# Optimization experiments

Measured on AMD Instinct MI355X. Metric: run time of the kernel, lower is better.

The kernel has to match this reference:

```python
import jax, jax.numpy as jnp
import numpy as np

BOUND = 2.0


def _near_far_cube(rays_o, rays_d, bound):
    tmin = (-bound - rays_o) / (rays_d + 1e-15)
    tmax = (bound - rays_o) / (rays_d + 1e-15)
    near = jnp.max(jnp.minimum(tmin, tmax), axis=-1, keepdims=True)
    far = jnp.min(jnp.maximum(tmin, tmax), axis=-1, keepdims=True)
    bad = far < near
    near = jnp.where(bad, 1e9, near)
    far = jnp.where(bad, 1e9, far)
    near = jnp.maximum(near, 0.05)
    return near, far


def _sample_pdf_det(bins, weights, n_samples):
    # bins: [R, M], weights: [R, M-1]  (deterministic / eval-mode u)
    weights = weights + 1e-5
    pdf = weights / jnp.sum(weights, -1, keepdims=True)
    cdf = jnp.cumsum(pdf, -1)
    cdf = jnp.concatenate([jnp.zeros_like(cdf[:, :1]), cdf], -1)  # [R, M]
    u = jnp.linspace(0.5 / n_samples, 1.0 - 0.5 / n_samples, n_samples, dtype=cdf.dtype)
    u = jnp.broadcast_to(u, (cdf.shape[0], n_samples))
    inds = jax.vmap(lambda c, uu: jnp.searchsorted(c, uu, side='right'))(cdf, u)
    below = jnp.maximum(inds - 1, 0)
    above = jnp.minimum(inds, cdf.shape[-1] - 1)
    cdf_b = jnp.take_along_axis(cdf, below, -1)
    cdf_a = jnp.take_along_axis(cdf, above, -1)
    bins_b = jnp.take_along_axis(bins, below, -1)
    bins_a = jnp.take_along_axis(bins, above, -1)
    denom = cdf_a - cdf_b
    denom = jnp.where(denom < 1e-5, jnp.ones_like(denom), denom)
    t = (u - cdf_b) / denom
    return bins_b + t * (bins_a - bins_b)


def _field(pts, dirs, W1, b1, W2, b2, Wsig, Wrgb, brgb):
    # stand-in NeRF field (base class is abstract): tiny MLP
    h = jax.nn.relu(pts @ W1 + b1)
    h = jax.nn.relu(h @ W2 + b2)
    sigma = jax.nn.softplus((h @ Wsig)[..., 0])
    rgb = jax.nn.sigmoid(jnp.concatenate([h, dirs], -1) @ Wrgb + brgb)
    return sigma, rgb


def _composite_weights(z_vals, sigmas, sample_dist):
    deltas = z_vals[..., 1:] - z_vals[..., :-1]
    deltas = jnp.concatenate([deltas, jnp.broadcast_to(sample_dist, deltas[..., :1].shape)], -1)
    alphas = 1.0 - jnp.exp(-deltas * sigmas)
    shifted = jnp.concatenate([jnp.ones_like(alphas[..., :1]), 1.0 - alphas + 1e-15], -1)
    weights = alphas * jnp.cumprod(shifted, -1)[..., :-1]
    return weights, deltas


def _run(rays_o, rays_d, W1, b1, W2, b2, Wsig, Wrgb, brgb, num_steps, upsample_steps):
    B, N = rays_o.shape[:2]
    near, far = _near_far_cube(rays_o, rays_d, BOUND)          # [B,N,1]
    z = jnp.linspace(0.0, 1.0, num_steps, dtype=rays_o.dtype)
    z_vals = near + (far - near) * z                            # [B,N,S]
    sample_dist = (far - near) / num_steps                      # [B,N,1]
    pts = jnp.clip(rays_o[..., None, :] + rays_d[..., None, :] * z_vals[..., None], -BOUND, BOUND)
    dirs = jnp.broadcast_to(rays_d[..., None, :], pts.shape)
    sigmas, rgbs = _field(pts, dirs, W1, b1, W2, b2, Wsig, Wrgb, brgb)  # [B,N,S], [B,N,S,3]

    # importance resampling (no_grad + detach in torch -> stop_gradient)
    w, deltas = _composite_weights(z_vals, sigmas, sample_dist)
    z_mid = z_vals[..., :-1] + 0.5 * deltas[..., :-1]           # [B,N,S-1]
    new_z = _sample_pdf_det(z_mid.reshape(B * N, -1), w.reshape(B * N, -1)[:, 1:-1], upsample_steps)
    new_z = jax.lax.stop_gradient(new_z).reshape(B, N, upsample_steps)
    new_pts = jnp.clip(rays_o[..., None, :] + rays_d[..., None, :] * new_z[..., None], -BOUND, BOUND)
    new_dirs = jnp.broadcast_to(rays_d[..., None, :], new_pts.shape)
    new_sigmas, new_rgbs = _field(new_pts, new_dirs, W1, b1, W2, b2, Wsig, Wrgb, brgb)

    # merge coarse + fine samples, sort along ray
    z_all = jnp.concatenate([z_vals, new_z], -1)                # [B,N,S+U]
    idx = jnp.argsort(z_all, axis=-1)
    z_all = jnp.take_along_axis(z_all, idx, -1)
    sig_all = jnp.take_along_axis(jnp.concatenate([sigmas, new_sigmas], -1), idx, -1)
    rgb_all = jnp.take_along_axis(jnp.concatenate([rgbs, new_rgbs], -2), idx[..., None], -2)

    w, _ = _composite_weights(z_all, sig_all, sample_dist)
    weights_sum = jnp.sum(w, -1)                                # [B,N]
    ori_z = jnp.clip((z_all - near) / (far - near), 0.0, 1.0)
    depth = jnp.sum(w * ori_z, -1)                              # [B,N]
    image = jnp.sum(w[..., None] * rgb_all, -2)                 # [B,N,3]
    image = image + (1.0 - weights_sum)[..., None] * 1.0        # bg_color = 1
    return depth, image


def setup_inputs() -> dict:
    key = jax.random.key(0)
    ks = jax.random.split(key, 8)
    B, N, H = 1, 4096, 64
    rays_o = jax.random.normal(ks[0], (B, N, 3), jnp.float32) * 0.5
    rays_d = jax.random.normal(ks[1], (B, N, 3), jnp.float32)
    rays_d = rays_d / jnp.linalg.norm(rays_d, axis=-1, keepdims=True)
    return {
        'rays_o': rays_o,
        'rays_d': rays_d,
        'W1': jax.random.normal(ks[2], (3, H), jnp.float32) / np.sqrt(3.0),
        'b1': jnp.zeros((H,), jnp.float32),
        'W2': jax.random.normal(ks[3], (H, H), jnp.float32) / np.sqrt(H),
        'b2': jnp.zeros((H,), jnp.float32),
        'Wsig': jax.random.normal(ks[4], (H, 1), jnp.float32) / np.sqrt(H),
        'Wrgb': jax.random.normal(ks[5], (H + 3, 3), jnp.float32) / np.sqrt(H + 3),
        'brgb': jnp.zeros((3,), jnp.float32),
        'num_steps': 128,
        'upsample_steps': 128,
    }


def reference(rays_o, rays_d, W1, b1, W2, b2, Wsig, Wrgb, brgb, num_steps, upsample_steps):
    return _run(rays_o, rays_d, W1, b1, W2, b2, Wsig, Wrgb, brgb, num_steps, upsample_steps)
```

## Files before the change

### kernel.cpp

```cpp
#include <hip/hip_runtime.h>
#include <math.h>


#define BOUNDF 2.0f

typedef _Float16 f16;
typedef f16 f16x2 __attribute__((ext_vector_type(2)));
typedef f16 f16x8 __attribute__((ext_vector_type(8)));
typedef float f32x4 __attribute__((ext_vector_type(4)));

union U16 { f16x8 v8; f16x2 v2[4]; };

struct RayLds {
    float zc[128];
    float zf[128];
    float sgc[128];
    float sgf[128];
    float rgbc[128][3];
    float rgbf[128][3];
    float cdf[128];
    float scr[128];
    unsigned short perm[256];
};

__device__ __forceinline__ f32x4 mfma16(f16x8 a, f16x8 b, f32x4 c) {
    return __builtin_amdgcn_mfma_f32_16x16x32_f16(a, b, c, 0, 0, 0);
}

__device__ __forceinline__ f16x2 pkrtz(float a, float b) {
    return __builtin_bit_cast(f16x2, __builtin_amdgcn_cvt_pkrtz(a, b));
}

__device__ __forceinline__ f16x8 relu_pk(f16x8 x) {
    const f16x8 z = {(f16)0.f, (f16)0.f, (f16)0.f, (f16)0.f,
                     (f16)0.f, (f16)0.f, (f16)0.f, (f16)0.f};
    return __builtin_elementwise_max(x, z);
}

__device__ __forceinline__ float scan_incl_mul(float p, int lane) {
#pragma unroll
    for (int off = 1; off < 64; off <<= 1) {
        float t = __shfl_up(p, off, 64);
        if (lane >= off) p *= t;
    }
    return p;
}

__device__ __forceinline__ float scan_incl_add(float p, int lane) {
#pragma unroll
    for (int off = 1; off < 64; off <<= 1) {
        float t = __shfl_up(p, off, 64);
        if (lane >= off) p += t;
    }
    return p;
}

template<bool COARSE>
__device__ __forceinline__ void field_pass(
    RayLds& R,
    f16x8 w1a0, f16x8 w1a1, f16x8 w1a2, f16x8 w1a3,
    f16x8 b00, f16x8 b01, f16x8 b10, f16x8 b11,
    f16x8 b20, f16x8 b21, f16x8 b30, f16x8 b31,
    f16x8 hda0, f16x8 hda1,
    f32x4 b2q0, f32x4 b2q1, f32x4 b2q2, f32x4 b2q3,
    float ox, float oy, float oz, float dx, float dy, float dzv,
    float nearv, float span, float base_r, float base_g, float base_b, int lane)
{
    const int ms = lane & 15;
    f32x4* stage = (f32x4*)(&R.cdf[0]);
    const f32x4 zero = {0.f, 0.f, 0.f, 0.f};
    U16 up;
    up.v2[2] = f16x2{(f16)0.f, (f16)0.f};
    up.v2[3] = f16x2{(f16)0.f, (f16)0.f};
#pragma unroll 1
    for (int Mtb = 0; Mtb < 2; ++Mtb) {
#pragma unroll 2
        for (int Mti = 0; Mti < 4; ++Mti) {
            int m = Mtb * 64 + Mti * 16 + ms;
            float z = COARSE ? fmaf(span, (float)m * (1.0f / 127.0f), nearv) : R.zf[m];
            float px = fminf(fmaxf(fmaf(dx, z, ox), -BOUNDF), BOUNDF);
            float py = fminf(fmaxf(fmaf(dy, z, oy), -BOUNDF), BOUNDF);
            float pz = fminf(fmaxf(fmaf(dzv, z, oz), -BOUNDF), BOUNDF);

            up.v2[0] = pkrtz(px, py);
            up.v2[1] = pkrtz(pz, 1.0f);
            f16x8 pf = up.v8;

            f32x4 hacc0 = mfma16(w1a0, pf, zero);
            f32x4 hacc1 = mfma16(w1a1, pf, zero);
            f32x4 hacc2 = mfma16(w1a2, pf, zero);
            f32x4 hacc3 = mfma16(w1a3, pf, zero);

            U16 u0, u1;
            u0.v2[0] = pkrtz(hacc0[0], hacc0[1]);
            u0.v2[1] = pkrtz(hacc0[2], hacc0[3]);
            u0.v2[2] = pkrtz(hacc1[0], hacc1[1]);
            u0.v2[3] = pkrtz(hacc1[2], hacc1[3]);
            u1.v2[0] = pkrtz(hacc2[0], hacc2[1]);
            u1.v2[1] = pkrtz(hacc2[2], hacc2[3]);
            u1.v2[2] = pkrtz(hacc3[0], hacc3[1]);
            u1.v2[3] = pkrtz(hacc3[2], hacc3[3]);
            f16x8 hf0 = relu_pk(u0.v8), hf1 = relu_pk(u1.v8);

            f32x4 acc0 = mfma16(b01, hf1, mfma16(b00, hf0, b2q0));
            f32x4 acc1 = mfma16(b11, hf1, mfma16(b10, hf0, b2q1));
            f32x4 acc2 = mfma16(b21, hf1, mfma16(b20, hf0, b2q2));
            f32x4 acc3 = mfma16(b31, hf1, mfma16(b30, hf0, b2q3));

            U16 v0, v1;
            v0.v2[0] = pkrtz(acc0[0], acc0[1]);
            v0.v2[1] = pkrtz(acc0[2], acc0[3]);
            v0.v2[2] = pkrtz(acc1[0], acc1[1]);
            v0.v2[3] = pkrtz(acc1[2], acc1[3]);
            v1.v2[0] = pkrtz(acc2[0], acc2[1]);
            v1.v2[1] = pkrtz(acc2[2], acc2[3]);
            v1.v2[2] = pkrtz(acc3[0], acc3[1]);
            v1.v2[3] = pkrtz(acc3[2], acc3[3]);
            f16x8 h0 = relu_pk(v0.v8), h1f = relu_pk(v1.v8);

            f32x4 tv = mfma16(hda1, h1f, mfma16(hda0, h0, zero));
            if (lane < 16) stage[Mti * 16 + ms] = tv;
        }
        {
            f32x4 tq = stage[lane];
            int m2 = Mtb * 64 + lane;
            float e  = __expf(-fabsf(tq[0]));
            float sg = fmaxf(tq[0], 0.0f) + __logf(1.0f + e);
            float rr = __builtin_amdgcn_rcpf(1.0f + __expf(-(tq[1] + base_r)));
            float gg = __builtin_amdgcn_rcpf(1.0f + __expf(-(tq[2] + base_g)));
            float bb = __builtin_amdgcn_rcpf(1.0f + __expf(-(tq[3] + base_b)));
            if (COARSE) {
                R.sgc[m2] = sg;
                R.rgbc[m2][0] = rr; R.rgbc[m2][1] = gg; R.rgbc[m2][2] = bb;
            } else {
                R.sgf[m2] = sg;
                R.rgbf[m2][0] = rr; R.rgbf[m2][1] = gg; R.rgbf[m2][2] = bb;
            }
        }
    }
}

__global__ __launch_bounds__(256)
void nerf_kernel(const float* __restrict__ rays_o, const float* __restrict__ rays_d,
                 const float* __restrict__ W1, const float* __restrict__ b1,
                 const float* __restrict__ W2, const float* __restrict__ b2,
                 const float* __restrict__ Wsig, const float* __restrict__ Wrgb,
                 const float* __restrict__ brgb,
                 float* __restrict__ out_depth, float* __restrict__ out_img,
                 int nRays)
{
    __shared__ RayLds rl[4];

    const int tid  = threadIdx.x;
    const int lane = tid & 63;
    const int wv   = tid >> 6;
    const int ms   = lane & 15;
    const int quad = lane >> 4;

    f16x8 w1a[4];
#pragma unroll
    for (int nt = 0; nt < 4; ++nt) {
        f16x8 t;
#pragma unroll
        for (int j = 0; j < 8; ++j) t[j] = (f16)0.f;
        if (quad == 0) {
            int u = 32 * (nt >> 1) + 8 * (ms >> 2) + 4 * (nt & 1) + (ms & 3);
            t[0] = (f16)W1[u];
            t[1] = (f16)W1[64 + u];
            t[2] = (f16)W1[128 + u];
            t[3] = (f16)b1[u];
        }
        w1a[nt] = t;
    }

    const int colbase = 8 * (ms >> 2) + (ms & 3);
    f16x8 b00, b01, b10, b11, b20, b21, b30, b31;
#pragma unroll
    for (int j = 0; j < 8; ++j) {
        int k0 = (quad * 8 + j) * 64;
        int k1 = (32 + quad * 8 + j) * 64;
        b00[j] = (f16)W2[k0 + colbase];      b01[j] = (f16)W2[k1 + colbase];
        b10[j] = (f16)W2[k0 + colbase + 4];  b11[j] = (f16)W2[k1 + colbase + 4];
        b20[j] = (f16)W2[k0 + colbase + 32]; b21[j] = (f16)W2[k1 + colbase + 32];
        b30[j] = (f16)W2[k0 + colbase + 36]; b31[j] = (f16)W2[k1 + colbase + 36];
    }
    f32x4 b2q0, b2q1, b2q2, b2q3;
#pragma unroll
    for (int r = 0; r < 4; ++r) {
        b2q0[r] = b2[8 * quad + r];
        b2q1[r] = b2[8 * quad + 4 + r];
        b2q2[r] = b2[32 + 8 * quad + r];
        b2q3[r] = b2[32 + 8 * quad + 4 + r];
    }
    f16x8 hda0, hda1;
    {
        int msel = ms & 3;
#pragma unroll
        for (int j = 0; j < 8; ++j) {
            int u0 = quad * 8 + j, u1 = 32 + quad * 8 + j;
            float w0 = (msel == 0) ? Wsig[u0] : Wrgb[u0 * 3 + msel - 1];
            float w1 = (msel == 0) ? Wsig[u1] : Wrgb[u1 * 3 + msel - 1];
            hda0[j] = (f16)w0;
            hda1[j] = (f16)w1;
        }
    }

    int ray = blockIdx.x * 4 + wv;
    bool valid = ray < nRays;
    int rayc = valid ? ray : (nRays - 1);
    RayLds& R = rl[wv];

    const float ox = rays_o[rayc * 3 + 0], oy = rays_o[rayc * 3 + 1], oz = rays_o[rayc * 3 + 2];
    const float dx = rays_d[rayc * 3 + 0], dy = rays_d[rayc * 3 + 1], dzv = rays_d[rayc * 3 + 2];

    float t0x = (-BOUNDF - ox) / (dx + 1e-15f), t1x = (BOUNDF - ox) / (dx + 1e-15f);
    float t0y = (-BOUNDF - oy) / (dy + 1e-15f), t1y = (BOUNDF - oy) / (dy + 1e-15f);
    float t0z = (-BOUNDF - oz) / (dzv + 1e-15f), t1z = (BOUNDF - oz) / (dzv + 1e-15f);
    float nearv = fmaxf(fminf(t0x, t1x), fmaxf(fminf(t0y, t1y), fminf(t0z, t1z)));
    float farv  = fminf(fmaxf(t0x, t1x), fminf(fmaxf(t0y, t1y), fmaxf(t0z, t1z)));
    if (farv < nearv) { nearv = 1e9f; farv = 1e9f; }
    nearv = fmaxf(nearv, 0.05f);
    const float span = farv - nearv;
    const float dzc = span * (1.0f / 127.0f);
    const float sample_dist = span * (1.0f / 128.0f);

    const float base_r = brgb[0] + dx * Wrgb[64 * 3 + 0] + dy * Wrgb[65 * 3 + 0] + dzv * Wrgb[66 * 3 + 0];
    const float base_g = brgb[1] + dx * Wrgb[64 * 3 + 1] + dy * Wrgb[65 * 3 + 1] + dzv * Wrgb[66 * 3 + 1];
    const float base_b = brgb[2] + dx * Wrgb[64 * 3 + 2] + dy * Wrgb[65 * 3 + 2] + dzv * Wrgb[66 * 3 + 2];

    const int s0 = lane, s1 = lane + 64;

    R.zc[s0] = fmaf(span, (float)s0 * (1.0f / 127.0f), nearv);
    R.zc[s1] = fmaf(span, (float)s1 * (1.0f / 127.0f), nearv);

    field_pass<true>(R, w1a[0], w1a[1], w1a[2], w1a[3],
                     b00, b01, b10, b11, b20, b21, b30, b31,
                     hda0, hda1, b2q0, b2q1, b2q2, b2q3,
                     ox, oy, oz, dx, dy, dzv, nearv, span, base_r, base_g, base_b, lane);

    {
        float zA = R.zc[s0], zB = R.zc[s1];
        float dA = R.zc[s0 + 1] - zA;
        float dB = (s1 < 127) ? (R.zc[s1 + 1] - zB) : sample_dist;
        R.scr[s0] = 1.0f - __expf(-dA * R.sgc[s0]);
        R.scr[s1] = 1.0f - __expf(-dB * R.sgc[s1]);
    }

    {
        float aa = R.scr[2 * lane], ab = R.scr[2 * lane + 1];
        float ma = 1.0f - aa + 1e-15f, mb = 1.0f - ab + 1e-15f;
        float p = scan_incl_mul(ma * mb, lane);
        float T0 = __shfl_up(p, 1, 64);
        if (lane == 0) T0 = 1.0f;
        R.scr[2 * lane]     = aa * T0;
        R.scr[2 * lane + 1] = ab * (T0 * ma);
    }

    {
        float pA = 0.f, pB = 0.f;
        if (lane < 63) {
            pA = R.scr[2 * lane + 1] + 1e-5f;
            pB = R.scr[2 * lane + 2] + 1e-5f;
        }
        float S = scan_incl_add(pA + pB, lane);
        float total = __shfl(S, 63, 64);
        float sexcl = __shfl_up(S, 1, 64);
        if (lane == 0) sexcl = 0.f;
        float inv = 1.0f / total;
        if (lane == 63) {
            R.cdf[0] = 0.0f;
        } else {
            R.cdf[1 + 2 * lane] = (sexcl + pA) * inv;
            R.cdf[2 + 2 * lane] = (sexcl + pA + pB) * inv;
        }
    }

#pragma unroll
    for (int bt = 0; bt < 2; ++bt) {
        int i = bt * 64 + lane;
        float u = (float)(2 * i + 1) * (1.0f / 256.0f);
        int lo = 0, hi = 127;
#pragma unroll
        for (int it = 0; it < 7; ++it) {
            int mid = (lo + hi) >> 1;
            if (R.cdf[mid] <= u) lo = mid + 1; else hi = mid;
        }
        int below = max(lo - 1, 0), above = min(lo, 126);
        float cb = R.cdf[below], ca = R.cdf[above];
        float binb = fmaf(dzc, (float)below + 0.5f, nearv);
        float bina = fmaf(dzc, (float)above + 0.5f, nearv);
        float denom = ca - cb;
        if (denom < 1e-5f) denom = 1.0f;
        float t = (u - cb) / denom;
        R.zf[i] = fmaf(t, bina - binb, binb);
    }

    field_pass<false>(R, w1a[0], w1a[1], w1a[2], w1a[3],
                      b00, b01, b10, b11, b20, b21, b30, b31,
                      hda0, hda1, b2q0, b2q1, b2q2, b2q3,
                      ox, oy, oz, dx, dy, dzv, nearv, span, base_r, base_g, base_b, lane);

#pragma unroll
    for (int bt = 0; bt < 2; ++bt) {
        int k = bt * 64 + lane;
        float v = R.zc[k];
        float vf = R.zf[k];
        int lo = 0, hi = 128;
        int lo2 = 0, hi2 = 128;
#pragma unroll
        for (int it = 0; it < 8; ++it) {
            if (lo < hi)   { int mid = (lo + hi) >> 1;   if (R.zf[mid] < v)   lo = mid + 1;  else hi = mid; }
            if (lo2 < hi2) { int mid = (lo2 + hi2) >> 1; if (R.zc[mid] <= vf) lo2 = mid + 1; else hi2 = mid; }
        }
        R.perm[k + lo]  = (unsigned short)k;
        R.perm[k + lo2] = (unsigned short)(128 + k);
    }

    {
        int sb = 4 * lane;
        int idxk[4]; float zk[4], sgk[4];
#pragma unroll
        for (int k = 0; k < 4; ++k) {
            int idx = R.perm[sb + k];
            idxk[k] = idx;
            zk[k]  = (idx < 128) ? R.zc[idx]  : R.zf[idx - 128];
            sgk[k] = (idx < 128) ? R.sgc[idx] : R.sgf[idx - 128];
        }
        float znext = __shfl_down(zk[0], 1, 64);
        float d0 = zk[1] - zk[0];
        float d1 = zk[2] - zk[1];
        float d2 = zk[3] - zk[2];
        float d3 = (lane < 63) ? (znext - zk[3]) : sample_dist;
        float a0 = 1.0f - __expf(-d0 * sgk[0]);
        float a1 = 1.0f - __expf(-d1 * sgk[1]);
        float a2 = 1.0f - __expf(-d2 * sgk[2]);
        float a3 = 1.0f - __expf(-d3 * sgk[3]);
        float m0 = 1.0f - a0 + 1e-15f, m1 = 1.0f - a1 + 1e-15f;
        float m2 = 1.0f - a2 + 1e-15f, m3 = 1.0f - a3 + 1e-15f;
        float p = scan_incl_mul((m0 * m1) * (m2 * m3), lane);
        float T = __shfl_up(p, 1, 64);
        if (lane == 0) T = 1.0f;

        const float invspan = 1.0f / span;
        float dacc = 0.f, racc = 0.f, gacc = 0.f, bacc = 0.f, wacc = 0.f;
        float aarr[4] = {a0, a1, a2, a3};
        float marr[4] = {m0, m1, m2, m3};
#pragma unroll
        for (int k = 0; k < 4; ++k) {
            float w = aarr[k] * T;
            float ozv = (zk[k] - nearv) * invspan;
            ozv = (ozv < 0.0f) ? 0.0f : ((ozv > 1.0f) ? 1.0f : ozv);
            dacc = fmaf(w, ozv, dacc);
            const float* rgb = (idxk[k] < 128) ? R.rgbc[idxk[k]] : R.rgbf[idxk[k] - 128];
            racc = fmaf(w, rgb[0], racc);
            gacc = fmaf(w, rgb[1], gacc);
            bacc = fmaf(w, rgb[2], bacc);
            wacc += w;
            T *= marr[k];
        }
#pragma unroll
        for (int off = 32; off; off >>= 1) {
            dacc += __shfl_xor(dacc, off);
            racc += __shfl_xor(racc, off);
            gacc += __shfl_xor(gacc, off);
            bacc += __shfl_xor(bacc, off);
            wacc += __shfl_xor(wacc, off);
        }
        if (lane == 0 && valid) {
            out_depth[ray] = dacc;
            float bg = 1.0f - wacc;
            out_img[ray * 3 + 0] = racc + bg;
            out_img[ray * 3 + 1] = gacc + bg;
            out_img[ray * 3 + 2] = bacc + bg;
        }
    }
}

extern "C" void kernel_launch(void* const* d_in, const int* in_sizes, int n_in,
                              void* d_out, int out_size, void* d_ws, size_t ws_size,
                              hipStream_t stream) {
    const float* rays_o = (const float*)d_in[0];
    const float* rays_d = (const float*)d_in[1];
    const float* W1   = (const float*)d_in[2];
    const float* b1   = (const float*)d_in[3];
    const float* W2   = (const float*)d_in[4];
    const float* b2   = (const float*)d_in[5];
    const float* Wsig = (const float*)d_in[6];
    const float* Wrgb = (const float*)d_in[7];
    const float* brgb = (const float*)d_in[8];

    int N = in_sizes[0] / 3;
    float* out = (float*)d_out;
    float* out_depth = out;
    float* out_img   = out + N;

    int blocks = (N + 3) / 4;
    nerf_kernel<<<dim3(blocks), dim3(256), 0, stream>>>(
        rays_o, rays_d, W1, b1, W2, b2, Wsig, Wrgb, brgb,
        out_depth, out_img, N);
}
```

Measured before the change: 98.59 us.

## Split each ray's field evaluation across two cooperating waves

Assigns two waves per ray instead of one. Each wave evaluates half of the coarse and fine MLP sample tiles, with block barriers before the stages that need all samples. Scan, CDF and composite stages are computed redundantly by both waves, with only one writing the output. This doubles wave-level parallelism to hide latency and raise occupancy, at the cost of duplicated serial work and extra barriers.

```diff
diff --git a/kernel.cpp b/kernel.cpp
--- a/kernel.cpp
+++ b/kernel.cpp
@@ -11,15 +11,17 @@
 
 union U16 { f16x8 v8; f16x2 v2[4]; };
 
-struct RayLds {
+struct __align__(16) RayLds {
     float zc[128];
     float zf[128];
     float sgc[128];
     float sgf[128];
     float rgbc[128][3];
     float rgbf[128][3];
+    float scr[128];
+    float wbuf[128];
     float cdf[128];
-    float scr[128];
+    float stg[512];
     unsigned short perm[256];
 };
 
@@ -57,7 +59,7 @@
 
 template<bool COARSE>
 __device__ __forceinline__ void field_pass(
-    RayLds& R,
+    RayLds& R, int mtb,
     f16x8 w1a0, f16x8 w1a1, f16x8 w1a2, f16x8 w1a3,
     f16x8 b00, f16x8 b01, f16x8 b10, f16x8 b11,
     f16x8 b20, f16x8 b21, f16x8 b30, f16x8 b31,
@@ -67,75 +69,73 @@
     float nearv, float span, float base_r, float base_g, float base_b, int lane)
 {
     const int ms = lane & 15;
-    f32x4* stage = (f32x4*)(&R.cdf[0]);
+    f32x4* stage = (f32x4*)(&R.stg[0]);
+    const int sb = mtb * 64;
     const f32x4 zero = {0.f, 0.f, 0.f, 0.f};
     U16 up;
     up.v2[2] = f16x2{(f16)0.f, (f16)0.f};
     up.v2[3] = f16x2{(f16)0.f, (f16)0.f};
-#pragma unroll 1
-    for (int Mtb = 0; Mtb < 2; ++Mtb) {
 #pragma unroll 2
-        for (int Mti = 0; Mti < 4; ++Mti) {
-            int m = Mtb * 64 + Mti * 16 + ms;
-            float z = COARSE ? fmaf(span, (float)m * (1.0f / 127.0f), nearv) : R.zf[m];
-            float px = fminf(fmaxf(fmaf(dx, z, ox), -BOUNDF), BOUNDF);
-            float py = fminf(fmaxf(fmaf(dy, z, oy), -BOUNDF), BOUNDF);
-            float pz = fminf(fmaxf(fmaf(dzv, z, oz), -BOUNDF), BOUNDF);
-
-            up.v2[0] = pkrtz(px, py);
-            up.v2[1] = pkrtz(pz, 1.0f);
-            f16x8 pf = up.v8;
-
-            f32x4 hacc0 = mfma16(w1a0, pf, zero);
-            f32x4 hacc1 = mfma16(w1a1, pf, zero);
-            f32x4 hacc2 = mfma16(w1a2, pf, zero);
-            f32x4 hacc3 = mfma16(w1a3, pf, zero);
-
-            U16 u0, u1;
-            u0.v2[0] = pkrtz(hacc0[0], hacc0[1]);
-            u0.v2[1] = pkrtz(hacc0[2], hacc0[3]);
-            u0.v2[2] = pkrtz(hacc1[0], hacc1[1]);
-            u0.v2[3] = pkrtz(hacc1[2], hacc1[3]);
-            u1.v2[0] = pkrtz(hacc2[0], hacc2[1]);
-            u1.v2[1] = pkrtz(hacc2[2], hacc2[3]);
-            u1.v2[2] = pkrtz(hacc3[0], hacc3[1]);
-            u1.v2[3] = pkrtz(hacc3[2], hacc3[3]);
-            f16x8 hf0 = relu_pk(u0.v8), hf1 = relu_pk(u1.v8);
-
-            f32x4 acc0 = mfma16(b01, hf1, mfma16(b00, hf0, b2q0));
-            f32x4 acc1 = mfma16(b11, hf1, mfma16(b10, hf0, b2q1));
-            f32x4 acc2 = mfma16(b21, hf1, mfma16(b20, hf0, b2q2));
-            f32x4 acc3 = mfma16(b31, hf1, mfma16(b30, hf0, b2q3));
-
-            U16 v0, v1;
-            v0.v2[0] = pkrtz(acc0[0], acc0[1]);
-            v0.v2[1] = pkrtz(acc0[2], acc0[3]);
-            v0.v2[2] = pkrtz(acc1[0], acc1[1]);
-            v0.v2[3] = pkrtz(acc1[2], acc1[3]);
-            v1.v2[0] = pkrtz(acc2[0], acc2[1]);
-            v1.v2[1] = pkrtz(acc2[2], acc2[3]);
-            v1.v2[2] = pkrtz(acc3[0], acc3[1]);
-            v1.v2[3] = pkrtz(acc3[2], acc3[3]);
-            f16x8 h0 = relu_pk(v0.v8), h1f = relu_pk(v1.v8);
-
-            f32x4 tv = mfma16(hda1, h1f, mfma16(hda0, h0, zero));
-            if (lane < 16) stage[Mti * 16 + ms] = tv;
-        }
-        {
-            f32x4 tq = stage[lane];
-            int m2 = Mtb * 64 + lane;
-            float e  = __expf(-fabsf(tq[0]));
-            float sg = fmaxf(tq[0], 0.0f) + __logf(1.0f + e);
-            float rr = __builtin_amdgcn_rcpf(1.0f + __expf(-(tq[1] + base_r)));
-            float gg = __builtin_amdgcn_rcpf(1.0f + __expf(-(tq[2] + base_g)));
-            float bb = __builtin_amdgcn_rcpf(1.0f + __expf(-(tq[3] + base_b)));
-            if (COARSE) {
-                R.sgc[m2] = sg;
-                R.rgbc[m2][0] = rr; R.rgbc[m2][1] = gg; R.rgbc[m2][2] = bb;
-            } else {
-                R.sgf[m2] = sg;
-                R.rgbf[m2][0] = rr; R.rgbf[m2][1] = gg; R.rgbf[m2][2] = bb;
-            }
+    for (int Mti = 0; Mti < 4; ++Mti) {
+        int m = sb + Mti * 16 + ms;
+        float z = COARSE ? fmaf(span, (float)m * (1.0f / 127.0f), nearv) : R.zf[m];
+        float px = fminf(fmaxf(fmaf(dx, z, ox), -BOUNDF), BOUNDF);
+        float py = fminf(fmaxf(fmaf(dy, z, oy), -BOUNDF), BOUNDF);
+        float pz = fminf(fmaxf(fmaf(dzv, z, oz), -BOUNDF), BOUNDF);
+
+        up.v2[0] = pkrtz(px, py);
+        up.v2[1] = pkrtz(pz, 1.0f);
+        f16x8 pf = up.v8;
+
+        f32x4 hacc0 = mfma16(w1a0, pf, zero);
+        f32x4 hacc1 = mfma16(w1a1, pf, zero);
+        f32x4 hacc2 = mfma16(w1a2, pf, zero);
+        f32x4 hacc3 = mfma16(w1a3, pf, zero);
+
+        U16 u0, u1;
+        u0.v2[0] = pkrtz(hacc0[0], hacc0[1]);
+        u0.v2[1] = pkrtz(hacc0[2], hacc0[3]);
+        u0.v2[2] = pkrtz(hacc1[0], hacc1[1]);
+        u0.v2[3] = pkrtz(hacc1[2], hacc1[3]);
+        u1.v2[0] = pkrtz(hacc2[0], hacc2[1]);
+        u1.v2[1] = pkrtz(hacc2[2], hacc2[3]);
+        u1.v2[2] = pkrtz(hacc3[0], hacc3[1]);
+        u1.v2[3] = pkrtz(hacc3[2], hacc3[3]);
+        f16x8 hf0 = relu_pk(u0.v8), hf1 = relu_pk(u1.v8);
+
+        f32x4 acc0 = mfma16(b01, hf1, mfma16(b00, hf0, b2q0));
+        f32x4 acc1 = mfma16(b11, hf1, mfma16(b10, hf0, b2q1));
+        f32x4 acc2 = mfma16(b21, hf1, mfma16(b20, hf0, b2q2));
+        f32x4 acc3 = mfma16(b31, hf1, mfma16(b30, hf0, b2q3));
+
+        U16 v0, v1;
+        v0.v2[0] = pkrtz(acc0[0], acc0[1]);
+        v0.v2[1] = pkrtz(acc0[2], acc0[3]);
+        v0.v2[2] = pkrtz(acc1[0], acc1[1]);
+        v0.v2[3] = pkrtz(acc1[2], acc1[3]);
+        v1.v2[0] = pkrtz(acc2[0], acc2[1]);
+        v1.v2[1] = pkrtz(acc2[2], acc2[3]);
+        v1.v2[2] = pkrtz(acc3[0], acc3[1]);
+        v1.v2[3] = pkrtz(acc3[2], acc3[3]);
+        f16x8 h0 = relu_pk(v0.v8), h1f = relu_pk(v1.v8);
+
+        f32x4 tv = mfma16(hda1, h1f, mfma16(hda0, h0, zero));
+        if (lane < 16) stage[sb + Mti * 16 + ms] = tv;
+    }
+    {
+        f32x4 tq = stage[sb + lane];
+        int m2 = sb + lane;
+        float e  = __expf(-fabsf(tq[0]));
+        float sg = fmaxf(tq[0], 0.0f) + __logf(1.0f + e);
+        float rr = __builtin_amdgcn_rcpf(1.0f + __expf(-(tq[1] + base_r)));
+        float gg = __builtin_amdgcn_rcpf(1.0f + __expf(-(tq[2] + base_g)));
+        float bb = __builtin_amdgcn_rcpf(1.0f + __expf(-(tq[3] + base_b)));
+        if (COARSE) {
+            R.sgc[m2] = sg;
+            R.rgbc[m2][0] = rr; R.rgbc[m2][1] = gg; R.rgbc[m2][2] = bb;
+        } else {
+            R.sgf[m2] = sg;
+            R.rgbf[m2][0] = rr; R.rgbf[m2][1] = gg; R.rgbf[m2][2] = bb;
         }
     }
 }
@@ -149,11 +149,13 @@
                  float* __restrict__ out_depth, float* __restrict__ out_img,
                  int nRays)
 {
-    __shared__ RayLds rl[4];
+    __shared__ RayLds rl[2];
 
     const int tid  = threadIdx.x;
     const int lane = tid & 63;
     const int wv   = tid >> 6;
+    const int p    = wv & 1;
+    const int pr   = wv >> 1;
     const int ms   = lane & 15;
     const int quad = lane >> 4;
 
@@ -205,10 +207,10 @@
         }
     }
 
-    int ray = blockIdx.x * 4 + wv;
+    int ray = blockIdx.x * 2 + pr;
     bool valid = ray < nRays;
     int rayc = valid ? ray : (nRays - 1);
-    RayLds& R = rl[wv];
+    RayLds& R = rl[pr];
 
     const float ox = rays_o[rayc * 3 + 0], oy = rays_o[rayc * 3 + 1], oz = rays_o[rayc * 3 + 2];
     const float dx = rays_d[rayc * 3 + 0], dy = rays_d[rayc * 3 + 1], dzv = rays_d[rayc * 3 + 2];
@@ -230,13 +232,17 @@
 
     const int s0 = lane, s1 = lane + 64;
 
-    R.zc[s0] = fmaf(span, (float)s0 * (1.0f / 127.0f), nearv);
-    R.zc[s1] = fmaf(span, (float)s1 * (1.0f / 127.0f), nearv);
-
-    field_pass<true>(R, w1a[0], w1a[1], w1a[2], w1a[3],
+    {
+        int i = p * 64 + lane;
+        R.zc[i] = fmaf(span, (float)i * (1.0f / 127.0f), nearv);
+    }
+
+    field_pass<true>(R, p, w1a[0], w1a[1], w1a[2], w1a[3],
                      b00, b01, b10, b11, b20, b21, b30, b31,
                      hda0, hda1, b2q0, b2q1, b2q2, b2q3,
                      ox, oy, oz, dx, dy, dzv, nearv, span, base_r, base_g, base_b, lane);
+
+    __syncthreads();
 
     {
         float zA = R.zc[s0], zB = R.zc[s1];
@@ -249,18 +255,18 @@
     {
         float aa = R.scr[2 * lane], ab = R.scr[2 * lane + 1];
         float ma = 1.0f - aa + 1e-15f, mb = 1.0f - ab + 1e-15f;
-        float p = scan_incl_mul(ma * mb, lane);
-        float T0 = __shfl_up(p, 1, 64);
+        float pp = scan_incl_mul(ma * mb, lane);
+        float T0 = __shfl_up(pp, 1, 64);
         if (lane == 0) T0 = 1.0f;
-        R.scr[2 * lane]     = aa * T0;
-        R.scr[2 * lane + 1] = ab * (T0 * ma);
+        R.wbuf[2 * lane]     = aa * T0;
+        R.wbuf[2 * lane + 1] = ab * (T0 * ma);
     }
 
     {
         float pA = 0.f, pB = 0.f;
         if (lane < 63) {
-            pA = R.scr[2 * lane + 1] + 1e-5f;
-            pB = R.scr[2 * lane + 2] + 1e-5f;
+            pA = R.wbuf[2 * lane + 1] + 1e-5f;
+            pB = R.wbuf[2 * lane + 2] + 1e-5f;
         }
         float S = scan_incl_add(pA + pB, lane);
         float total = __shfl(S, 63, 64);
@@ -275,9 +281,8 @@
         }
     }
 
-#pragma unroll
-    for (int bt = 0; bt < 2; ++bt) {
-        int i = bt * 64 + lane;
+    {
+        int i = p * 64 + lane;
         float u = (float)(2 * i + 1) * (1.0f / 256.0f);
         int lo = 0, hi = 127;
 #pragma unroll
@@ -295,14 +300,15 @@
         R.zf[i] = fmaf(t, bina - binb, binb);
     }
 
-    field_pass<false>(R, w1a[0], w1a[1], w1a[2], w1a[3],
+    field_pass<false>(R, p, w1a[0], w1a[1], w1a[2], w1a[3],
                       b00, b01, b10, b11, b20, b21, b30, b31,
                       hda0, hda1, b2q0, b2q1, b2q2, b2q3,
                       ox, oy, oz, dx, dy, dzv, nearv, span, base_r, base_g, base_b, lane);
 
-#pragma unroll
-    for (int bt = 0; bt < 2; ++bt) {
-        int k = bt * 64 + lane;
+    __syncthreads();
+
+    {
+        int k = p * 64 + lane;
         float v = R.zc[k];
         float vf = R.zf[k];
         int lo = 0, hi = 128;
@@ -315,6 +321,8 @@
         R.perm[k + lo]  = (unsigned short)k;
         R.perm[k + lo2] = (unsigned short)(128 + k);
     }
+
+    __syncthreads();
 
     {
         int sb = 4 * lane;
@@ -337,8 +345,8 @@
         float a3 = 1.0f - __expf(-d3 * sgk[3]);
         float m0 = 1.0f - a0 + 1e-15f, m1 = 1.0f - a1 + 1e-15f;
         float m2 = 1.0f - a2 + 1e-15f, m3 = 1.0f - a3 + 1e-15f;
-        float p = scan_incl_mul((m0 * m1) * (m2 * m3), lane);
-        float T = __shfl_up(p, 1, 64);
+        float pp = scan_incl_mul((m0 * m1) * (m2 * m3), lane);
+        float T = __shfl_up(pp, 1, 64);
         if (lane == 0) T = 1.0f;
 
         const float invspan = 1.0f / span;
@@ -366,7 +374,7 @@
             bacc += __shfl_xor(bacc, off);
             wacc += __shfl_xor(wacc, off);
         }
-        if (lane == 0 && valid) {
+        if (lane == 0 && p == 0 && valid) {
             out_depth[ray] = dacc;
             float bg = 1.0f - wacc;
             out_img[ray * 3 + 0] = racc + bg;
@@ -394,7 +402,7 @@
     float* out_depth = out;
     float* out_img   = out + N;
 
-    int blocks = (N + 3) / 4;
+    int blocks = (N + 1) / 2;
     nerf_kernel<<<dim3(blocks), dim3(256), 0, stream>>>(
         rays_o, rays_d, W1, b1, W2, b2, Wsig, Wrgb, brgb,
         out_depth, out_img, N);
```

After: 104.4 us. +5.8%, slower.

## Pack rgb+sigma into f32x4 LDS records and recompute coarse z analytically

Applied to the files above, without the earlier changes.

Restructures the per-ray LDS layout so each sample stores rgb and sigma as one 16-byte vector, which turns scattered scalar LDS reads and writes into single vector accesses. Coarse z values are recomputed from near/span instead of being stored, and the coarse weight and pdf computation now stays in registers using shuffles instead of LDS scratch round trips. The inner field loop is fully unrolled. The staging buffer grows, so LDS use per block rises, and the extra unrolling may add register pressure.

```diff
diff --git a/kernel.cpp b/kernel.cpp
--- a/kernel.cpp
+++ b/kernel.cpp
@@ -11,15 +11,12 @@
 
 union U16 { f16x8 v8; f16x2 v2[4]; };
 
-struct RayLds {
-    float zc[128];
+struct __align__(16) RayLds {
     float zf[128];
-    float sgc[128];
-    float sgf[128];
-    float rgbc[128][3];
-    float rgbf[128][3];
     float cdf[128];
-    float scr[128];
+    f32x4 rgbc4[128];
+    f32x4 rgbf4[128];
+    f32x4 stg[128];
     unsigned short perm[256];
 };
 
@@ -67,14 +64,13 @@
     float nearv, float span, float base_r, float base_g, float base_b, int lane)
 {
     const int ms = lane & 15;
-    f32x4* stage = (f32x4*)(&R.cdf[0]);
     const f32x4 zero = {0.f, 0.f, 0.f, 0.f};
     U16 up;
     up.v2[2] = f16x2{(f16)0.f, (f16)0.f};
     up.v2[3] = f16x2{(f16)0.f, (f16)0.f};
 #pragma unroll 1
     for (int Mtb = 0; Mtb < 2; ++Mtb) {
-#pragma unroll 2
+#pragma unroll
         for (int Mti = 0; Mti < 4; ++Mti) {
             int m = Mtb * 64 + Mti * 16 + ms;
             float z = COARSE ? fmaf(span, (float)m * (1.0f / 127.0f), nearv) : R.zf[m];
@@ -119,23 +115,18 @@
             f16x8 h0 = relu_pk(v0.v8), h1f = relu_pk(v1.v8);
 
             f32x4 tv = mfma16(hda1, h1f, mfma16(hda0, h0, zero));
-            if (lane < 16) stage[Mti * 16 + ms] = tv;
+            if (lane < 16) R.stg[Mtb * 64 + Mti * 16 + ms] = tv;
         }
         {
-            f32x4 tq = stage[lane];
+            f32x4 tq = R.stg[Mtb * 64 + lane];
             int m2 = Mtb * 64 + lane;
             float e  = __expf(-fabsf(tq[0]));
             float sg = fmaxf(tq[0], 0.0f) + __logf(1.0f + e);
             float rr = __builtin_amdgcn_rcpf(1.0f + __expf(-(tq[1] + base_r)));
             float gg = __builtin_amdgcn_rcpf(1.0f + __expf(-(tq[2] + base_g)));
             float bb = __builtin_amdgcn_rcpf(1.0f + __expf(-(tq[3] + base_b)));
-            if (COARSE) {
-                R.sgc[m2] = sg;
-                R.rgbc[m2][0] = rr; R.rgbc[m2][1] = gg; R.rgbc[m2][2] = bb;
-            } else {
-                R.sgf[m2] = sg;
-                R.rgbf[m2][0] = rr; R.rgbf[m2][1] = gg; R.rgbf[m2][2] = bb;
-            }
+            f32x4 o = {rr, gg, bb, sg};
+            if (COARSE) R.rgbc4[m2] = o; else R.rgbf4[m2] = o;
         }
     }
 }
@@ -228,40 +219,27 @@
     const float base_g = brgb[1] + dx * Wrgb[64 * 3 + 1] + dy * Wrgb[65 * 3 + 1] + dzv * Wrgb[66 * 3 + 1];
     const float base_b = brgb[2] + dx * Wrgb[64 * 3 + 2] + dy * Wrgb[65 * 3 + 2] + dzv * Wrgb[66 * 3 + 2];
 
-    const int s0 = lane, s1 = lane + 64;
-
-    R.zc[s0] = fmaf(span, (float)s0 * (1.0f / 127.0f), nearv);
-    R.zc[s1] = fmaf(span, (float)s1 * (1.0f / 127.0f), nearv);
-
     field_pass<true>(R, w1a[0], w1a[1], w1a[2], w1a[3],
                      b00, b01, b10, b11, b20, b21, b30, b31,
                      hda0, hda1, b2q0, b2q1, b2q2, b2q3,
                      ox, oy, oz, dx, dy, dzv, nearv, span, base_r, base_g, base_b, lane);
 
     {
-        float zA = R.zc[s0], zB = R.zc[s1];
-        float dA = R.zc[s0 + 1] - zA;
-        float dB = (s1 < 127) ? (R.zc[s1 + 1] - zB) : sample_dist;
-        R.scr[s0] = 1.0f - __expf(-dA * R.sgc[s0]);
-        R.scr[s1] = 1.0f - __expf(-dB * R.sgc[s1]);
-    }
-
-    {
-        float aa = R.scr[2 * lane], ab = R.scr[2 * lane + 1];
-        float ma = 1.0f - aa + 1e-15f, mb = 1.0f - ab + 1e-15f;
-        float p = scan_incl_mul(ma * mb, lane);
-        float T0 = __shfl_up(p, 1, 64);
+        float sgA = R.rgbc4[2 * lane][3];
+        float sgB = R.rgbc4[2 * lane + 1][3];
+        float aA = 1.0f - __expf(-dzc * sgA);
+        float dB = (lane == 63) ? sample_dist : dzc;
+        float aB = 1.0f - __expf(-dB * sgB);
+        float mA = 1.0f - aA + 1e-15f, mB = 1.0f - aB + 1e-15f;
+        float pp = scan_incl_mul(mA * mB, lane);
+        float T0 = __shfl_up(pp, 1, 64);
         if (lane == 0) T0 = 1.0f;
-        R.scr[2 * lane]     = aa * T0;
-        R.scr[2 * lane + 1] = ab * (T0 * ma);
-    }
-
-    {
-        float pA = 0.f, pB = 0.f;
-        if (lane < 63) {
-            pA = R.scr[2 * lane + 1] + 1e-5f;
-            pB = R.scr[2 * lane + 2] + 1e-5f;
-        }
+        float w0 = aA * T0;
+        float w1 = aB * (T0 * mA);
+        float w2n = __shfl_down(w0, 1, 64);
+        float pA = w1 + 1e-5f;
+        float pB = w2n + 1e-5f;
+        if (lane == 63) { pA = 0.f; pB = 0.f; }
         float S = scan_incl_add(pA + pB, lane);
         float total = __shfl(S, 63, 64);
         float sexcl = __shfl_up(S, 1, 64);
@@ -303,14 +281,21 @@
 #pragma unroll
     for (int bt = 0; bt < 2; ++bt) {
         int k = bt * 64 + lane;
-        float v = R.zc[k];
+        float v  = fmaf(span, (float)k * (1.0f / 127.0f), nearv);
         float vf = R.zf[k];
         int lo = 0, hi = 128;
         int lo2 = 0, hi2 = 128;
 #pragma unroll
         for (int it = 0; it < 8; ++it) {
-            if (lo < hi)   { int mid = (lo + hi) >> 1;   if (R.zf[mid] < v)   lo = mid + 1;  else hi = mid; }
-            if (lo2 < hi2) { int mid = (lo2 + hi2) >> 1; if (R.zc[mid] <= vf) lo2 = mid + 1; else hi2 = mid; }
+            if (lo < hi) {
+                int mid = (lo + hi) >> 1;
+                if (R.zf[mid] < v) lo = mid + 1; else hi = mid;
+            }
+            if (lo2 < hi2) {
+                int mid = (lo2 + hi2) >> 1;
+                float zcm = fmaf(span, (float)mid * (1.0f / 127.0f), nearv);
+                if (zcm <= vf) lo2 = mid + 1; else hi2 = mid;
+            }
         }
         R.perm[k + lo]  = (unsigned short)k;
         R.perm[k + lo2] = (unsigned short)(128 + k);
@@ -318,23 +303,26 @@
 
     {
         int sb = 4 * lane;
-        int idxk[4]; float zk[4], sgk[4];
+        int idxk[4]; float zk[4]; f32x4 ck[4];
 #pragma unroll
         for (int k = 0; k < 4; ++k) {
             int idx = R.perm[sb + k];
             idxk[k] = idx;
-            zk[k]  = (idx < 128) ? R.zc[idx]  : R.zf[idx - 128];
-            sgk[k] = (idx < 128) ? R.sgc[idx] : R.sgf[idx - 128];
+            float zfv = R.zf[idx & 127];
+            float zcv = fmaf(span, (float)idx * (1.0f / 127.0f), nearv);
+            zk[k] = (idx < 128) ? zcv : zfv;
+            const f32x4* src = (idx < 128) ? &R.rgbc4[idx] : &R.rgbf4[idx - 128];
+            ck[k] = *src;
         }
         float znext = __shfl_down(zk[0], 1, 64);
         float d0 = zk[1] - zk[0];
         float d1 = zk[2] - zk[1];
         float d2 = zk[3] - zk[2];
         float d3 = (lane < 63) ? (znext - zk[3]) : sample_dist;
-        float a0 = 1.0f - __expf(-d0 * sgk[0]);
-        float a1 = 1.0f - __expf(-d1 * sgk[1]);
-        float a2 = 1.0f - __expf(-d2 * sgk[2]);
-        float a3 = 1.0f - __expf(-d3 * sgk[3]);
+        float a0 = 1.0f - __expf(-d0 * ck[0][3]);
+        float a1 = 1.0f - __expf(-d1 * ck[1][3]);
+        float a2 = 1.0f - __expf(-d2 * ck[2][3]);
+        float a3 = 1.0f - __expf(-d3 * ck[3][3]);
         float m0 = 1.0f - a0 + 1e-15f, m1 = 1.0f - a1 + 1e-15f;
         float m2 = 1.0f - a2 + 1e-15f, m3 = 1.0f - a3 + 1e-15f;
         float p = scan_incl_mul((m0 * m1) * (m2 * m3), lane);
@@ -351,10 +339,9 @@
             float ozv = (zk[k] - nearv) * invspan;
             ozv = (ozv < 0.0f) ? 0.0f : ((ozv > 1.0f) ? 1.0f : ozv);
             dacc = fmaf(w, ozv, dacc);
-            const float* rgb = (idxk[k] < 128) ? R.rgbc[idxk[k]] : R.rgbf[idxk[k] - 128];
-            racc = fmaf(w, rgb[0], racc);
-            gacc = fmaf(w, rgb[1], gacc);
-            bacc = fmaf(w, rgb[2], bacc);
+            racc = fmaf(w, ck[k][0], racc);
+            gacc = fmaf(w, ck[k][1], gacc);
+            bacc = fmaf(w, ck[k][2], bacc);
             wacc += w;
             T *= marr[k];
         }
```

Result: no change. 97.58 us (-1.0%).
